# Optimization experiments

Hardware: AMD Instinct MI355X
Metric: run time of the kernel (lower is better)

Reference implementation:

```python
import jax, jax.numpy as jnp
import numpy as np

B, I, H = 16384, 512, 512
HH = H // 2


def _lrelu(v):
    return jnp.where(v > 0, v, 0.01 * v)


def setup_inputs() -> dict:
    key = jax.random.key(0)
    ks = jax.random.split(key, 20)
    s = 1.0 / np.sqrt(H)
    rn = lambda k, shp, sc: (jax.random.normal(k, shp, jnp.float32) * sc)
    return {
        "x": rn(ks[0], (B, I), 1.0),
        "h0": rn(ks[1], (1, B, H), 1.0),
        "c0": rn(ks[2], (1, B, H), 1.0),
        "cum": jax.random.uniform(ks[3], (B, 1), jnp.float32),
        # LSTM params (torch gate order i, f, g, o)
        "W_ih": rn(ks[4], (4 * H, I), s),
        "W_hh": rn(ks[5], (4 * H, H), s),
        "b_ih": rn(ks[6], (4 * H,), s),
        "b_hh": rn(ks[7], (4 * H,), s),
        # skip gate MLP
        "W_sp": rn(ks[8], (HH, H), s),
        "b_sp": rn(ks[9], (HH,), s),
        "W_sc": rn(ks[10], (HH, H), s),
        "b_sc": rn(ks[11], (HH,), s),
        "W_so": rn(ks[12], (1, HH), s),
        "b_so": rn(ks[13], (1,), s),
        # threshold gate MLP
        "W_tp": rn(ks[14], (HH, H), s),
        "b_tp": rn(ks[15], (HH,), s),
        "W_to": rn(ks[16], (1, HH), s),
        "b_to": rn(ks[17], (1,), s),
    }


def reference(x, h0, c0, cum, W_ih, W_hh, b_ih, b_hh,
              W_sp, b_sp, W_sc, b_sc, W_so, b_so,
              W_tp, b_tp, W_to, b_to):
    # single-step, single-layer LSTM
    gates = x @ W_ih.T + b_ih + h0[0] @ W_hh.T + b_hh  # [B, 4H]
    i_g, f_g, g_g, o_g = jnp.split(gates, 4, axis=-1)
    i_g = jax.nn.sigmoid(i_g)
    f_g = jax.nn.sigmoid(f_g)
    g_g = jnp.tanh(g_g)
    o_g = jax.nn.sigmoid(o_g)
    c1l = f_g * c0[0] + i_g * g_g          # [B, H]
    h1l = o_g * jnp.tanh(c1l)              # [B, H]
    h1, c1 = h1l[None], c1l[None]          # [1, B, H]

    # skip gate: delta prob from c0[-1], c1[-1]
    sg = _lrelu(c0[-1] @ W_sp.T + b_sp + c1[-1] @ W_sc.T + b_sc)  # [B, H/2]
    update_prob_delta = jax.nn.sigmoid(sg @ W_so.T + b_so)        # [B, 1]

    # threshold gate from c0[-1]
    tg = _lrelu(c0[-1] @ W_tp.T + b_tp)                           # [B, H/2]
    update_threshold = jax.nn.sigmoid(tg @ W_to.T + b_to)         # [B, 1]

    update_prob = cum + jnp.minimum(update_prob_delta, 1.0 - cum)  # [B, 1]
    # straight-through round: fwd hard threshold, bwd identity to prob
    hard = (update_prob > update_threshold).astype(jnp.float32)
    update_gate = update_prob + jax.lax.stop_gradient(hard - update_prob)

    new_h = update_gate * h1 + (1.0 - update_gate) * h0  # [1, B, H]
    new_c = update_gate * c1 + (1.0 - update_gate) * c0  # [1, B, H]
    update_cum = (1.0 - update_gate) * update_prob        # [B, 1]
    return (new_h, new_c, update_cum, update_prob_delta, update_prob)
```

## Files before the change

### kernel.cpp

```cpp
#include <hip/hip_runtime.h>
#include <math.h>

#define BB 16384
#define HH 512

typedef short short8 __attribute__((ext_vector_type(8)));
typedef float f32x4 __attribute__((ext_vector_type(4)));
typedef unsigned short ushort_t;

__device__ __forceinline__ float sigm(float v){ return 1.0f/(1.0f+expf(-v)); }

__device__ __forceinline__ unsigned short f2bf(float f){
    unsigned int u = __float_as_uint(f);
    u = u + 0x7FFFu + ((u>>16)&1u);
    return (unsigned short)(u>>16);
}
__device__ __forceinline__ float bf2f(unsigned short h){
    return __uint_as_float(((unsigned int)h)<<16);
}
__device__ __forceinline__ void gll16(const void* g, void* l){
    __builtin_amdgcn_global_load_lds((const __attribute__((address_space(1))) void*)g,
                                     (__attribute__((address_space(3))) void*)l, 16, 0, 0);
}
__device__ __forceinline__ void split_store(float v, ushort_t* ph, ushort_t* pl, int j){
    unsigned short h = f2bf(v);
    unsigned short l = f2bf(v - bf2f(h));
    ph[j] = h; pl[j] = l;
}

__global__ void k_prep_all(
    const float* __restrict__ x, const float* __restrict__ h0, const float* __restrict__ c0,
    const float* __restrict__ W_ih, const float* __restrict__ W_hh,
    const float* __restrict__ b_ih, const float* __restrict__ b_hh,
    const float* __restrict__ W_sp, const float* __restrict__ W_sc, const float* __restrict__ W_tp,
    const float* __restrict__ b_sp, const float* __restrict__ b_sc, const float* __restrict__ b_tp,
    ushort_t* __restrict__ A1h, ushort_t* __restrict__ A1l,
    ushort_t* __restrict__ A2h, ushort_t* __restrict__ A2l,
    ushort_t* __restrict__ B1h, ushort_t* __restrict__ B1l,
    ushort_t* __restrict__ B2h, ushort_t* __restrict__ B2l,
    float* __restrict__ bgp, float* __restrict__ bs2)
{
    int bid = blockIdx.x;
    if (bid < 8192) {
        int u = bid*256 + threadIdx.x;
        int r  = u & 255;
        int c  = (u >> 8) & 3;
        int kt = (u >> 10) & 31;
        int tm = u >> 15;
        int row = tm*256 + r;
        int k0 = kt*32 + c*8;
        const float* src = (k0 < 512) ? (x + (size_t)row*512 + k0)
                                      : (h0 + (size_t)row*512 + (k0-512));
        float4 v0 = *(const float4*)(src);
        float4 v1 = *(const float4*)(src+4);
        float vv[8] = {v0.x,v0.y,v0.z,v0.w,v1.x,v1.y,v1.z,v1.w};
        size_t off = (size_t)u * 8;
#pragma unroll
        for (int j=0;j<8;++j) split_store(vv[j], A1h+off, A1l+off, j);
    } else if (bid < 12288) {
        int u = (bid-8192)*256 + threadIdx.x;
        int r  = u & 127;
        int c  = (u >> 7) & 3;
        int tk = (u >> 9) & 15;
        int tm = u >> 13;
        int row = tm*128 + r;
        int k0 = tk*32 + c*8;
        const float* src = c0 + (size_t)row*512 + k0;
        float4 v0 = *(const float4*)(src);
        float4 v1 = *(const float4*)(src+4);
        float vv[8] = {v0.x,v0.y,v0.z,v0.w,v1.x,v1.y,v1.z,v1.w};
        size_t off = ((size_t)tm*32 + tk)*4096 + (size_t)(c*128 + r)*8;
#pragma unroll
        for (int j=0;j<8;++j) split_store(vv[j], A2h+off, A2l+off, j);
    } else if (bid < 13312) {
        int u = (bid-12288)*256 + threadIdx.x;
        int r  = u & 255;
        int c  = (u >> 8) & 3;
        int kt = (u >> 10) & 31;
        int tn = u >> 15;
        int g = (r>>4)&3;
        int h = tn*64 + (r>>6)*16 + (r&15);
        int wrow = g*512 + h;
        int k0 = kt*32 + c*8;
        const float* src = (k0 < 512) ? (W_ih + (size_t)wrow*512 + k0)
                                      : (W_hh + (size_t)wrow*512 + (k0-512));
        float4 v0 = *(const float4*)(src);
        float4 v1 = *(const float4*)(src+4);
        float vv[8] = {v0.x,v0.y,v0.z,v0.w,v1.x,v1.y,v1.z,v1.w};
        size_t off = (size_t)u * 8;
#pragma unroll
        for (int j=0;j<8;++j) split_store(vv[j], B1h+off, B1l+off, j);
        if (kt == 0 && c == 0) bgp[tn*256 + r] = b_ih[wrow] + b_hh[wrow];
    } else {
        int u = (bid-13312)*256 + threadIdx.x;
        int r  = u & 127;
        int c  = (u >> 7) & 3;
        int tk = (u >> 9) & 31;
        int tn = u >> 14;
        int n = tn*128 + r;
        int k0 = tk*32 + c*8;
        float vv[8];
        if (n < 256) {
            const float* src = (k0 < 512) ? (W_sp + (size_t)n*512 + k0)
                                          : (W_sc + (size_t)n*512 + (k0-512));
            float4 v0 = *(const float4*)(src);
            float4 v1 = *(const float4*)(src+4);
            vv[0]=v0.x; vv[1]=v0.y; vv[2]=v0.z; vv[3]=v0.w;
            vv[4]=v1.x; vv[5]=v1.y; vv[6]=v1.z; vv[7]=v1.w;
        } else if (k0 < 512) {
            const float* src = W_tp + (size_t)(n-256)*512 + k0;
            float4 v0 = *(const float4*)(src);
            float4 v1 = *(const float4*)(src+4);
            vv[0]=v0.x; vv[1]=v0.y; vv[2]=v0.z; vv[3]=v0.w;
            vv[4]=v1.x; vv[5]=v1.y; vv[6]=v1.z; vv[7]=v1.w;
        } else {
#pragma unroll
            for (int j=0;j<8;++j) vv[j] = 0.0f;
        }
        size_t off = (size_t)u * 8;
#pragma unroll
        for (int j=0;j<8;++j) split_store(vv[j], B2h+off, B2l+off, j);
        if (tk == 0 && c == 0) bs2[n] = (n < 256) ? (b_sp[n] + b_sc[n]) : b_tp[n-256];
    }
}

#define STEPG(T, DO_STAGE, VMASM)                                                    \
  {                                                                                  \
    ushort_t* bufA = &lds[(T) & 3][0];                                               \
    ushort_t* bufB = &lds[(T) & 3][8192];                                            \
    short8 af[8], bf[4];                                                             \
    _Pragma("unroll") for (int f = 0; f < 8; ++f)                                    \
        af[f] = *(const short8*)&bufA[aoff[f]];                                      \
    _Pragma("unroll") for (int f = 0; f < 4; ++f)                                    \
        bf[f] = *(const short8*)&bufB[boff[f]];                                      \
    if (DO_STAGE) {                                                                  \
        const int uu = (T) + 3;                                                      \
        const ushort_t* As_ = ((uu >> 5) == 1) ? Al : Ah;                            \
        const ushort_t* Bs_ = ((uu >> 5) == 2) ? Bl : Bh;                            \
        size_t ga = ((size_t)tm*32 + (uu & 31))*8192 + (size_t)tid*8;                \
        size_t gb = ((size_t)tn*32 + (uu & 31))*8192 + (size_t)tid*8;                \
        ushort_t* dA = &lds[uu & 3][0];                                              \
        ushort_t* dB = &lds[uu & 3][8192];                                           \
        gll16(As_ + ga,        dA + tid*8);                                          \
        gll16(As_ + ga + 4096, dA + 4096 + tid*8);                                   \
        gll16(Bs_ + gb,        dB + tid*8);                                          \
        gll16(Bs_ + gb + 4096, dB + 4096 + tid*8);                                   \
    }                                                                                \
    VMASM;                                                                           \
    asm volatile("s_barrier" ::: "memory");                                          \
    asm volatile("s_waitcnt lgkmcnt(0)" ::: "memory");                               \
    __builtin_amdgcn_sched_barrier(0);                                               \
    __builtin_amdgcn_s_setprio(1);                                                   \
    _Pragma("unroll") for (int fm = 0; fm < 8; ++fm)                                 \
        _Pragma("unroll") for (int fn = 0; fn < 4; ++fn)                             \
            acc[fm][fn] = __builtin_amdgcn_mfma_f32_16x16x32_bf16(af[fm], bf[fn], acc[fm][fn], 0,0,0); \
    __builtin_amdgcn_s_setprio(0);                                                   \
    asm volatile("s_barrier" ::: "memory");                                          \
  }

__global__ __launch_bounds__(512, 2) void k_gemm_gates(
    const ushort_t* __restrict__ Ah, const ushort_t* __restrict__ Al,
    const ushort_t* __restrict__ Bh, const ushort_t* __restrict__ Bl,
    const float* __restrict__ bgp, const float* __restrict__ c0,
    float* __restrict__ outH, float* __restrict__ outC,
    ushort_t* __restrict__ A2h, ushort_t* __restrict__ A2l)
{
    __shared__ __align__(16) ushort_t lds[4][16384];
    const int tid  = threadIdx.x;
    const int lane = tid & 63;
    const int wid  = tid >> 6;
    const int wr   = wid >> 2;
    const int wc   = wid & 3;
    const int l15  = lane & 15;
    const int lq   = lane >> 4;
    const int bid  = (int)blockIdx.x;
    const int v    = (bid & 7)*64 + (bid >> 3);
    const int tm   = v >> 3;
    const int tn   = v & 7;

    f32x4 acc[8][4];
#pragma unroll
    for (int fn = 0; fn < 4; ++fn) {
        float bv = bgp[tn*256 + wc*64 + fn*16 + l15];
#pragma unroll
        for (int fm = 0; fm < 8; ++fm) {
            acc[fm][fn][0]=bv; acc[fm][fn][1]=bv; acc[fm][fn][2]=bv; acc[fm][fn][3]=bv;
        }
    }

    int aoff[8], boff[4];
#pragma unroll
    for (int f = 0; f < 8; ++f) aoff[f] = (lq*256 + wr*128 + f*16 + l15) * 8;
#pragma unroll
    for (int f = 0; f < 4; ++f) boff[f] = (lq*256 + wc*64 + f*16 + l15) * 8;

#pragma unroll
    for (int u0 = 0; u0 < 3; ++u0) {
        size_t ga = ((size_t)tm*32 + u0)*8192 + (size_t)tid*8;
        size_t gb = ((size_t)tn*32 + u0)*8192 + (size_t)tid*8;
        gll16(Ah + ga,        &lds[u0][0]     + tid*8);
        gll16(Ah + ga + 4096, &lds[u0][4096]  + tid*8);
        gll16(Bh + gb,        &lds[u0][8192]  + tid*8);
        gll16(Bh + gb + 4096, &lds[u0][12288] + tid*8);
    }
    asm volatile("s_waitcnt vmcnt(8)" ::: "memory");
    asm volatile("s_barrier" ::: "memory");

    for (int t = 0; t < 93; ++t) {
        STEPG(t, 1, asm volatile("s_waitcnt vmcnt(8)" ::: "memory"));
    }
    STEPG(93, 0, asm volatile("s_waitcnt vmcnt(4)" ::: "memory"));
    STEPG(94, 0, asm volatile("s_waitcnt vmcnt(0)" ::: "memory"));
    STEPG(95, 0, ((void)0));

    const int h = tn*64 + wc*16 + l15;
#pragma unroll
    for (int fm = 0; fm < 8; ++fm) {
        int row0 = tm*256 + wr*128 + fm*16 + lq*4;
#pragma unroll
        for (int r = 0; r < 4; ++r) {
            int row = row0 + r;
            size_t idx = (size_t)row*512 + h;
            float ig = sigm(acc[fm][0][r]);
            float fg = sigm(acc[fm][1][r]);
            float gg = tanhf(acc[fm][2][r]);
            float og = sigm(acc[fm][3][r]);
            float c1 = fg*c0[idx] + ig*gg;
            float h1 = og*tanhf(c1);
            outC[idx] = c1;
            outH[idx] = h1;
            unsigned short ch = f2bf(c1);
            unsigned short cl = f2bf(c1 - bf2f(ch));
            size_t a2 = ((size_t)(row>>7)*32 + 16 + (h>>5))*4096
                      + (size_t)((((h>>3)&3))*128 + (row&127))*8 + (h&7);
            A2h[a2] = ch;
            A2l[a2] = cl;
        }
    }
}

#define STEPS(T, DO_STAGE, VMASM)                                                    \
  {                                                                                  \
    ushort_t* bufA = &lds2[(T) & 3][0];                                              \
    ushort_t* bufB = &lds2[(T) & 3][4096];                                           \
    short8 af[4], bf[4];                                                             \
    _Pragma("unroll") for (int f = 0; f < 4; ++f)                                    \
        af[f] = *(const short8*)&bufA[aoff[f]];                                      \
    _Pragma("unroll") for (int f = 0; f < 4; ++f)                                    \
        bf[f] = *(const short8*)&bufB[boff[f]];                                      \
    if (DO_STAGE) {                                                                  \
        const int uu = (T) + 3;                                                      \
        const ushort_t* As_ = ((uu >> 5) == 1) ? Al : Ah;                            \
        const ushort_t* Bs_ = ((uu >> 5) == 2) ? Bl : Bh;                            \
        size_t ga = ((size_t)tm*32 + (uu & 31))*4096 + (size_t)tid*8;                \
        size_t gb = ((size_t)tn*32 + (uu & 31))*4096 + (size_t)tid*8;                \
        ushort_t* dA = &lds2[uu & 3][0];                                             \
        ushort_t* dB = &lds2[uu & 3][4096];                                          \
        gll16(As_ + ga,        dA + tid*8);                                          \
        gll16(As_ + ga + 2048, dA + 2048 + tid*8);                                   \
        gll16(Bs_ + gb,        dB + tid*8);                                          \
        gll16(Bs_ + gb + 2048, dB + 2048 + tid*8);                                   \
    }                                                                                \
    VMASM;                                                                           \
    asm volatile("s_barrier" ::: "memory");                                          \
    asm volatile("s_waitcnt lgkmcnt(0)" ::: "memory");                               \
    __builtin_amdgcn_sched_barrier(0);                                               \
    __builtin_amdgcn_s_setprio(1);                                                   \
    _Pragma("unroll") for (int fm = 0; fm < 4; ++fm)                                 \
        _Pragma("unroll") for (int fn = 0; fn < 4; ++fn)                             \
            acc[fm][fn] = __builtin_amdgcn_mfma_f32_16x16x32_bf16(af[fm], bf[fn], acc[fm][fn], 0,0,0); \
    __builtin_amdgcn_s_setprio(0);                                                   \
    asm volatile("s_barrier" ::: "memory");                                          \
  }

__global__ __launch_bounds__(256, 2) void k_gemm_sgtg(
    const ushort_t* __restrict__ Ah, const ushort_t* __restrict__ Al,
    const ushort_t* __restrict__ Bh, const ushort_t* __restrict__ Bl,
    const float* __restrict__ bs2,
    float* __restrict__ sgtg)
{
    __shared__ __align__(16) ushort_t lds2[4][8192];
    const int tid  = threadIdx.x;
    const int lane = tid & 63;
    const int wid  = tid >> 6;
    const int wr   = wid >> 1;
    const int wc   = wid & 1;
    const int l15  = lane & 15;
    const int lq   = lane >> 4;
    const int bid  = (int)blockIdx.x;
    const int v    = (bid & 7)*64 + (bid >> 3);
    const int tm   = v >> 2;
    const int tn   = v & 3;

    f32x4 acc[4][4];
#pragma unroll
    for (int fn = 0; fn < 4; ++fn) {
        float bv = bs2[tn*128 + wc*64 + fn*16 + l15];
#pragma unroll
        for (int fm = 0; fm < 4; ++fm) {
            acc[fm][fn][0]=bv; acc[fm][fn][1]=bv; acc[fm][fn][2]=bv; acc[fm][fn][3]=bv;
        }
    }

    int aoff[4], boff[4];
#pragma unroll
    for (int f = 0; f < 4; ++f) {
        aoff[f] = (lq*128 + wr*64 + f*16 + l15) * 8;
        boff[f] = (lq*128 + wc*64 + f*16 + l15) * 8;
    }

#pragma unroll
    for (int u0 = 0; u0 < 3; ++u0) {
        size_t ga = ((size_t)tm*32 + u0)*4096 + (size_t)tid*8;
        size_t gb = ((size_t)tn*32 + u0)*4096 + (size_t)tid*8;
        gll16(Ah + ga,        &lds2[u0][0]    + tid*8);
        gll16(Ah + ga + 2048, &lds2[u0][2048] + tid*8);
        gll16(Bh + gb,        &lds2[u0][4096] + tid*8);
        gll16(Bh + gb + 2048, &lds2[u0][6144] + tid*8);
    }
    asm volatile("s_waitcnt vmcnt(8)" ::: "memory");
    asm volatile("s_barrier" ::: "memory");

    for (int t = 0; t < 93; ++t) {
        STEPS(t, 1, asm volatile("s_waitcnt vmcnt(8)" ::: "memory"));
    }
    STEPS(93, 0, asm volatile("s_waitcnt vmcnt(4)" ::: "memory"));
    STEPS(94, 0, asm volatile("s_waitcnt vmcnt(0)" ::: "memory"));
    STEPS(95, 0, ((void)0));

#pragma unroll
    for (int fm = 0; fm < 4; ++fm) {
        int row0 = tm*128 + wr*64 + fm*16 + lq*4;
#pragma unroll
        for (int fn = 0; fn < 4; ++fn) {
            int n = tn*128 + wc*64 + fn*16 + l15;
#pragma unroll
            for (int r = 0; r < 4; ++r) {
                int row = row0 + r;
                float vv = acc[fm][fn][r];
                vv = vv > 0.f ? vv : 0.01f*vv;
                sgtg[(size_t)row*512 + n] = vv;
            }
        }
    }
}

__global__ __launch_bounds__(256) void k_final(
    const float* __restrict__ sgtg,
    const float* __restrict__ h0, const float* __restrict__ c0,
    const float* __restrict__ cum,
    const float* __restrict__ W_so, const float* __restrict__ b_so,
    const float* __restrict__ W_to, const float* __restrict__ b_to,
    float* __restrict__ outH, float* __restrict__ outC,
    float* __restrict__ outCum, float* __restrict__ outDelta, float* __restrict__ outProb)
{
    int w = threadIdx.x >> 6;
    int lane = threadIdx.x & 63;
    int b = blockIdx.x * 4 + w;
    const float* row = sgtg + (size_t)b * 512;
    float so = 0.f, to = 0.f;
#pragma unroll
    for (int u = 0; u < 4; ++u) {
        int c = lane + 64 * u;
        so = fmaf(row[c], W_so[c], so);
        to = fmaf(row[256 + c], W_to[c], to);
    }
#pragma unroll
    for (int off = 32; off; off >>= 1) {
        so += __shfl_down(so, off);
        to += __shfl_down(to, off);
    }
    so = __shfl(so, 0);
    to = __shfl(to, 0);
    float delta = sigm(so + b_so[0]);
    float thr   = sigm(to + b_to[0]);
    float cu = cum[b];
    float prob = cu + fminf(delta, 1.0f - cu);
    float hard = (prob > thr) ? 1.0f : 0.0f;
    if (lane == 0) {
        outDelta[b] = delta;
        outProb[b]  = prob;
        outCum[b]   = (1.0f - hard) * prob;
    }
    if (hard == 0.0f) {
#pragma unroll
        for (int u = 0; u < 8; ++u) {
            size_t idx = (size_t)b * 512 + lane + 64 * u;
            outH[idx] = h0[idx];
            outC[idx] = c0[idx];
        }
    }
}

extern "C" void kernel_launch(void* const* d_in, const int* in_sizes, int n_in,
                              void* d_out, int out_size, void* d_ws, size_t ws_size,
                              hipStream_t stream)
{
    const float* x    = (const float*)d_in[0];
    const float* h0   = (const float*)d_in[1];
    const float* c0   = (const float*)d_in[2];
    const float* cum  = (const float*)d_in[3];
    const float* W_ih = (const float*)d_in[4];
    const float* W_hh = (const float*)d_in[5];
    const float* b_ih = (const float*)d_in[6];
    const float* b_hh = (const float*)d_in[7];
    const float* W_sp = (const float*)d_in[8];
    const float* b_sp = (const float*)d_in[9];
    const float* W_sc = (const float*)d_in[10];
    const float* b_sc = (const float*)d_in[11];
    const float* W_so = (const float*)d_in[12];
    const float* b_so = (const float*)d_in[13];
    const float* W_tp = (const float*)d_in[14];
    const float* b_tp = (const float*)d_in[15];
    const float* W_to = (const float*)d_in[16];
    const float* b_to = (const float*)d_in[17];

    float* out      = (float*)d_out;
    float* outH     = out;
    float* outC     = out + (size_t)BB * HH;
    float* outCum   = out + (size_t)2 * BB * HH;
    float* outDelta = outCum + BB;
    float* outProb  = outDelta + BB;

    char* w = (char*)d_ws;
    ushort_t* A1h = (ushort_t*)(w);
    ushort_t* A1l = (ushort_t*)(w + 33554432ull);
    ushort_t* A2h = (ushort_t*)(w + 67108864ull);
    ushort_t* A2l = (ushort_t*)(w + 100663296ull);
    ushort_t* B1h = (ushort_t*)(w + 134217728ull);
    ushort_t* B1l = (ushort_t*)(w + 138412032ull);
    ushort_t* B2h = (ushort_t*)(w + 142606336ull);
    ushort_t* B2l = (ushort_t*)(w + 143654912ull);
    float*    bgp = (float*)(w + 144703488ull);
    float*    bs2 = (float*)(w + 144711680ull);
    float*    sgtg = (float*)A1h;

    k_prep_all<<<13568, 256, 0, stream>>>(x, h0, c0, W_ih, W_hh, b_ih, b_hh,
                                          W_sp, W_sc, W_tp, b_sp, b_sc, b_tp,
                                          A1h, A1l, A2h, A2l, B1h, B1l, B2h, B2l,
                                          bgp, bs2);
    k_gemm_gates<<<512, 512, 0, stream>>>(A1h, A1l, B1h, B1l, bgp, c0,
                                          outH, outC, A2h, A2l);
    k_gemm_sgtg<<<512, 256, 0, stream>>>(A2h, A2l, B2h, B2l, bs2, sgtg);
    k_final<<<4096, 256, 0, stream>>>(sgtg, h0, c0, cum, W_so, b_so, W_to, b_to,
                                      outH, outC, outCum, outDelta, outProb);
}
```

Baseline: 350.9 us.

## Double-buffer LDS fragment reads in registers to overlap with MFMA

```diff
diff --git a/kernel.cpp b/kernel.cpp
--- a/kernel.cpp
+++ b/kernel.cpp
@@ -124,15 +124,16 @@
     }
 }
 
-#define STEPG(T, DO_STAGE, VMASM)                                                    \
+#define GSTEP(T, CA, CB, NA, NB, DO_READS, DO_STAGE, VMASM)                          \
   {                                                                                  \
-    ushort_t* bufA = &lds[(T) & 3][0];                                               \
-    ushort_t* bufB = &lds[(T) & 3][8192];                                            \
-    short8 af[8], bf[4];                                                             \
-    _Pragma("unroll") for (int f = 0; f < 8; ++f)                                    \
-        af[f] = *(const short8*)&bufA[aoff[f]];                                      \
-    _Pragma("unroll") for (int f = 0; f < 4; ++f)                                    \
-        bf[f] = *(const short8*)&bufB[boff[f]];                                      \
+    if (DO_READS) {                                                                  \
+        const ushort_t* bufA1 = &lds[((T)+1) & 3][0];                                \
+        const ushort_t* bufB1 = &lds[((T)+1) & 3][8192];                             \
+        _Pragma("unroll") for (int f = 0; f < 8; ++f)                                \
+            NA[f] = *(const short8*)&bufA1[aoff[f]];                                 \
+        _Pragma("unroll") for (int f = 0; f < 4; ++f)                                \
+            NB[f] = *(const short8*)&bufB1[boff[f]];                                 \
+    }                                                                                \
     if (DO_STAGE) {                                                                  \
         const int uu = (T) + 3;                                                      \
         const ushort_t* As_ = ((uu >> 5) == 1) ? Al : Ah;                            \
@@ -146,15 +147,15 @@
         gll16(Bs_ + gb,        dB + tid*8);                                          \
         gll16(Bs_ + gb + 4096, dB + 4096 + tid*8);                                   \
     }                                                                                \
-    VMASM;                                                                           \
-    asm volatile("s_barrier" ::: "memory");                                          \
-    asm volatile("s_waitcnt lgkmcnt(0)" ::: "memory");                               \
     __builtin_amdgcn_sched_barrier(0);                                               \
     __builtin_amdgcn_s_setprio(1);                                                   \
     _Pragma("unroll") for (int fm = 0; fm < 8; ++fm)                                 \
         _Pragma("unroll") for (int fn = 0; fn < 4; ++fn)                             \
-            acc[fm][fn] = __builtin_amdgcn_mfma_f32_16x16x32_bf16(af[fm], bf[fn], acc[fm][fn], 0,0,0); \
+            acc[fm][fn] = __builtin_amdgcn_mfma_f32_16x16x32_bf16(CA[fm], CB[fn], acc[fm][fn], 0,0,0); \
     __builtin_amdgcn_s_setprio(0);                                                   \
+    asm volatile("s_waitcnt lgkmcnt(0)" ::: "memory");                               \
+    __builtin_amdgcn_sched_barrier(0);                                               \
+    VMASM;                                                                           \
     asm volatile("s_barrier" ::: "memory");                                          \
   }
 
@@ -194,6 +195,8 @@
 #pragma unroll
     for (int f = 0; f < 4; ++f) boff[f] = (lq*256 + wc*64 + f*16 + l15) * 8;
 
+    short8 a0[8], b0[4], a1[8], b1[4];
+
 #pragma unroll
     for (int u0 = 0; u0 < 3; ++u0) {
         size_t ga = ((size_t)tm*32 + u0)*8192 + (size_t)tid*8;
@@ -203,15 +206,23 @@
         gll16(Bh + gb,        &lds[u0][8192]  + tid*8);
         gll16(Bh + gb + 4096, &lds[u0][12288] + tid*8);
     }
-    asm volatile("s_waitcnt vmcnt(8)" ::: "memory");
+    asm volatile("s_waitcnt vmcnt(4)" ::: "memory");
     asm volatile("s_barrier" ::: "memory");
-
-    for (int t = 0; t < 93; ++t) {
-        STEPG(t, 1, asm volatile("s_waitcnt vmcnt(8)" ::: "memory"));
-    }
-    STEPG(93, 0, asm volatile("s_waitcnt vmcnt(4)" ::: "memory"));
-    STEPG(94, 0, asm volatile("s_waitcnt vmcnt(0)" ::: "memory"));
-    STEPG(95, 0, ((void)0));
+#pragma unroll
+    for (int f = 0; f < 8; ++f) a0[f] = *(const short8*)&lds[0][aoff[f]];
+#pragma unroll
+    for (int f = 0; f < 4; ++f) b0[f] = *(const short8*)&lds[0][8192 + boff[f]];
+    asm volatile("s_waitcnt lgkmcnt(0)" ::: "memory");
+    __builtin_amdgcn_sched_barrier(0);
+
+    for (int t = 0; t < 92; t += 2) {
+        GSTEP(t,   a0, b0, a1, b1, 1, 1, asm volatile("s_waitcnt vmcnt(4)" ::: "memory"));
+        GSTEP(t+1, a1, b1, a0, b0, 1, 1, asm volatile("s_waitcnt vmcnt(4)" ::: "memory"));
+    }
+    GSTEP(92, a0, b0, a1, b1, 1, 1, asm volatile("s_waitcnt vmcnt(4)" ::: "memory"));
+    GSTEP(93, a1, b1, a0, b0, 1, 0, asm volatile("s_waitcnt vmcnt(0)" ::: "memory"));
+    GSTEP(94, a0, b0, a1, b1, 1, 0, ((void)0));
+    GSTEP(95, a1, b1, a0, b0, 0, 0, ((void)0));
 
     const int h = tn*64 + wc*16 + l15;
 #pragma unroll
@@ -239,15 +250,16 @@
     }
 }
 
-#define STEPS(T, DO_STAGE, VMASM)                                                    \
+#define SSTEP(T, CA, CB, NA, NB, DO_READS, DO_STAGE, VMASM)                          \
   {                                                                                  \
-    ushort_t* bufA = &lds2[(T) & 3][0];                                              \
-    ushort_t* bufB = &lds2[(T) & 3][4096];                                           \
-    short8 af[4], bf[4];                                                             \
-    _Pragma("unroll") for (int f = 0; f < 4; ++f)                                    \
-        af[f] = *(const short8*)&bufA[aoff[f]];                                      \
-    _Pragma("unroll") for (int f = 0; f < 4; ++f)                                    \
-        bf[f] = *(const short8*)&bufB[boff[f]];                                      \
+    if (DO_READS) {                                                                  \
+        const ushort_t* bufA1 = &lds2[((T)+1) & 3][0];                               \
+        const ushort_t* bufB1 = &lds2[((T)+1) & 3][4096];                            \
+        _Pragma("unroll") for (int f = 0; f < 4; ++f)                                \
+            NA[f] = *(const short8*)&bufA1[aoff[f]];                                 \
+        _Pragma("unroll") for (int f = 0; f < 4; ++f)                                \
+            NB[f] = *(const short8*)&bufB1[boff[f]];                                 \
+    }                                                                                \
     if (DO_STAGE) {                                                                  \
         const int uu = (T) + 3;                                                      \
         const ushort_t* As_ = ((uu >> 5) == 1) ? Al : Ah;                            \
@@ -261,15 +273,15 @@
         gll16(Bs_ + gb,        dB + tid*8);                                          \
         gll16(Bs_ + gb + 2048, dB + 2048 + tid*8);                                   \
     }                                                                                \
-    VMASM;                                                                           \
-    asm volatile("s_barrier" ::: "memory");                                          \
-    asm volatile("s_waitcnt lgkmcnt(0)" ::: "memory");                               \
     __builtin_amdgcn_sched_barrier(0);                                               \
     __builtin_amdgcn_s_setprio(1);                                                   \
     _Pragma("unroll") for (int fm = 0; fm < 4; ++fm)                                 \
         _Pragma("unroll") for (int fn = 0; fn < 4; ++fn)                             \
-            acc[fm][fn] = __builtin_amdgcn_mfma_f32_16x16x32_bf16(af[fm], bf[fn], acc[fm][fn], 0,0,0); \
+            acc[fm][fn] = __builtin_amdgcn_mfma_f32_16x16x32_bf16(CA[fm], CB[fn], acc[fm][fn], 0,0,0); \
     __builtin_amdgcn_s_setprio(0);                                                   \
+    asm volatile("s_waitcnt lgkmcnt(0)" ::: "memory");                               \
+    __builtin_amdgcn_sched_barrier(0);                                               \
+    VMASM;                                                                           \
     asm volatile("s_barrier" ::: "memory");                                          \
   }
 
@@ -309,6 +321,8 @@
         boff[f] = (lq*128 + wc*64 + f*16 + l15) * 8;
     }
 
+    short8 a0[4], b0[4], a1[4], b1[4];
+
 #pragma unroll
     for (int u0 = 0; u0 < 3; ++u0) {
         size_t ga = ((size_t)tm*32 + u0)*4096 + (size_t)tid*8;
@@ -318,15 +332,23 @@
         gll16(Bh + gb,        &lds2[u0][4096] + tid*8);
         gll16(Bh + gb + 2048, &lds2[u0][6144] + tid*8);
     }
-    asm volatile("s_waitcnt vmcnt(8)" ::: "memory");
+    asm volatile("s_waitcnt vmcnt(4)" ::: "memory");
     asm volatile("s_barrier" ::: "memory");
-
-    for (int t = 0; t < 93; ++t) {
-        STEPS(t, 1, asm volatile("s_waitcnt vmcnt(8)" ::: "memory"));
-    }
-    STEPS(93, 0, asm volatile("s_waitcnt vmcnt(4)" ::: "memory"));
-    STEPS(94, 0, asm volatile("s_waitcnt vmcnt(0)" ::: "memory"));
-    STEPS(95, 0, ((void)0));
+#pragma unroll
+    for (int f = 0; f < 4; ++f) a0[f] = *(const short8*)&lds2[0][aoff[f]];
+#pragma unroll
+    for (int f = 0; f < 4; ++f) b0[f] = *(const short8*)&lds2[0][4096 + boff[f]];
+    asm volatile("s_waitcnt lgkmcnt(0)" ::: "memory");
+    __builtin_amdgcn_sched_barrier(0);
+
+    for (int t = 0; t < 92; t += 2) {
+        SSTEP(t,   a0, b0, a1, b1, 1, 1, asm volatile("s_waitcnt vmcnt(4)" ::: "memory"));
+        SSTEP(t+1, a1, b1, a0, b0, 1, 1, asm volatile("s_waitcnt vmcnt(4)" ::: "memory"));
+    }
+    SSTEP(92, a0, b0, a1, b1, 1, 1, asm volatile("s_waitcnt vmcnt(4)" ::: "memory"));
+    SSTEP(93, a1, b1, a0, b0, 1, 0, asm volatile("s_waitcnt vmcnt(0)" ::: "memory"));
+    SSTEP(94, a0, b0, a1, b1, 1, 0, ((void)0));
+    SSTEP(95, a1, b1, a0, b0, 0, 0, ((void)0));
 
 #pragma unroll
     for (int fm = 0; fm < 4; ++fm) {
```

After: 340.0 us. -3.1%, faster.
